# Optimization experiments

Hardware: AMD Instinct MI355X
Metric: run time of the kernel (lower is better)

The kernel has to match this reference:

```python
import jax, jax.numpy as jnp
import numpy as np


def setup_inputs() -> dict:
    key = jax.random.key(0)
    kq, kk = jax.random.split(key)
    B, Q, K, D = 32, 512, 512, 1024
    queries = jax.random.normal(kq, (B, Q, D), dtype=jnp.float32)
    keys = jax.random.normal(kk, (B, K, D), dtype=jnp.float32)
    # ProbabilityConverter learned scalars (is_temperature=True, is_bias=True)
    temperature = jnp.ones((), dtype=jnp.float32)
    bias = jnp.zeros((), dtype=jnp.float32)
    return {"queries": queries, "keys": keys, "temperature": temperature, "bias": bias}


def reference(queries, keys, temperature, bias):
    # Dot scoring: (B, Q, D) x (B, K, D) -> (B, Q, K)
    logits = jnp.einsum("bqd,bkd->bqk", queries, keys)
    # keys.eq(0.0)[:, :, :1].transpose(1, 2): mask positions where first key feature == 0
    key_mask = (keys[:, :, 0] == 0.0)[:, None, :]  # (B, 1, K)
    neg_inf = jnp.array(-jnp.inf, dtype=logits.dtype)
    logits = jnp.where(key_mask, neg_inf, logits)
    # confidence = sigmoid((logsumexp(logits) + bias) * temperature)
    approx_max_logit = jax.nn.logsumexp(logits, axis=-1)  # (B, Q)
    confidence = jax.nn.sigmoid((approx_max_logit + bias) * temperature)
    attn = jax.nn.softmax(logits, axis=-1)  # (B, Q, K)
    return attn, confidence
```

## Files before the change

### kernel.cpp

```cpp
#include <hip/hip_runtime.h>
#include <math.h>
#include <stdint.h>


#define NB 32
#define NQ 512
#define NK 512
#define ND 1024
#define BK 32
#define NT (ND / BK)
#define BM1 64
#define BM4 64
#define TILE_BYTES 65536
#define WS_TILES ((size_t)NB * NT * TILE_BYTES)
#define WS_TOTAL (WS_TILES + (size_t)NB * NK * 4)

typedef __attribute__((ext_vector_type(8))) short short8;
typedef __attribute__((ext_vector_type(4))) float f32x4;

__device__ __forceinline__ void bf_split(float x, unsigned& hbits, float& lo) {
  unsigned u = __float_as_uint(x);
  unsigned r = u + 0x7fffu + ((u >> 16) & 1u);
  hbits = r & 0xffff0000u;
  lo = x - __uint_as_float(hbits);
}
__device__ __forceinline__ unsigned pack_rn(float x0, float x1) {
  unsigned u0 = __float_as_uint(x0), u1 = __float_as_uint(x1);
  unsigned r0 = u0 + 0x7fffu + ((u0 >> 16) & 1u);
  unsigned r1 = u1 + 0x7fffu + ((u1 >> 16) & 1u);
  return (r0 >> 16) | (r1 & 0xffff0000u);
}

__device__ __forceinline__ int lds_off_write(int r, int c4) {
  int slot = ((c4 >> 1) + (r >> 1)) & 3;
  return r * 32 + slot * 8 + (c4 & 1) * 4;
}
__device__ __forceinline__ int lds_off_read(int r, int quad) {
  int slot = (quad + (r >> 1)) & 3;
  return r * 32 + slot * 8;
}

__global__ __launch_bounds__(256)
void convert_k(const float* __restrict__ Kg, unsigned char* __restrict__ ws) {
  const int bx = blockIdx.x;
  const int batch = bx >> 5, kt = bx & 31;
  const float* src = Kg + (size_t)batch * NK * ND + kt * BK;
  unsigned short* hiB = (unsigned short*)(ws + (size_t)bx * TILE_BYTES);
  unsigned short* loB = hiB + 32768 / 2;
  float* maskB = (float*)(ws + WS_TILES) + batch * NK;

#pragma unroll
  for (int i = 0; i < 16; ++i) {
    int idx = threadIdx.x + 256 * i;
    int c = idx >> 3, c4 = idx & 7;
    float4 v = *(const float4*)(src + (size_t)c * ND + c4 * 4);
    unsigned h0, h1, h2, h3;
    float l0, l1, l2, l3;
    bf_split(v.x, h0, l0); bf_split(v.y, h1, l1);
    bf_split(v.z, h2, l2); bf_split(v.w, h3, l3);
    int off = c * 32 + c4 * 4;
    *(uint2*)(&hiB[off]) = make_uint2((h0 >> 16) | h1, (h2 >> 16) | h3);
    *(uint2*)(&loB[off]) = make_uint2(pack_rn(l0, l1), pack_rn(l2, l3));
    if (kt == 0 && c4 == 0) maskB[c] = v.x;
  }
}

__device__ __forceinline__ void stage_a(unsigned short* hiA, unsigned short* loA,
                                        int ar, int ac4, float4 v) {
  unsigned h0, h1, h2, h3;
  float l0, l1, l2, l3;
  bf_split(v.x, h0, l0); bf_split(v.y, h1, l1);
  bf_split(v.z, h2, l2); bf_split(v.w, h3, l3);
  int off = lds_off_write(ar, ac4);
  *(uint2*)(&hiA[off]) = make_uint2((h0 >> 16) | h1, (h2 >> 16) | h3);
  *(uint2*)(&loA[off]) = make_uint2(pack_rn(l0, l1), pack_rn(l2, l3));
}

#define MFMA_BF16 __builtin_amdgcn_mfma_f32_16x16x32_bf16

#define BODY(KT, CURB, NXTB, CUR, NXT)                                         \
  do {                                                                         \
    short8 ahi[4], alo[4];                                                     \
    _Pragma("unroll") for (int mt = 0; mt < 4; ++mt) {                         \
      int off = lds_off_read(mt * 16 + ln15, quad);                            \
      ahi[mt] = *(const short8*)(&sAhi[CUR][off]);                             \
      alo[mt] = *(const short8*)(&sAlo[CUR][off]);                             \
    }                                                                          \
    if ((KT) + 1 < NT) {                                                       \
      const unsigned char* tb = wsB + (size_t)((KT) + 1) * TILE_BYTES;         \
      _Pragma("unroll") for (int nt = 0; nt < 4; ++nt) {                       \
        NXTB[2 * nt]     = *(const float4*)(tb + nt * 1024 + boff);            \
        NXTB[2 * nt + 1] = *(const float4*)(tb + 32768 + nt * 1024 + boff);    \
      }                                                                        \
      stage_a(sAhi[NXT], sAlo[NXT], ar, ac4, pa);                              \
      if ((KT) + 2 < NT)                                                       \
        pa = *(const float4*)(Qp + ((KT) + 2) * BK + (size_t)ar * ND + ac4 * 4);\
    }                                                                          \
    _Pragma("unroll") for (int nt = 0; nt < 4; ++nt) {                         \
      short8 bhi = *(const short8*)(&CURB[2 * nt]);                            \
      short8 blo = *(const short8*)(&CURB[2 * nt + 1]);                        \
      _Pragma("unroll") for (int mt = 0; mt < 4; ++mt) {                       \
        acc[mt][nt] = MFMA_BF16(ahi[mt], bhi, acc[mt][nt], 0, 0, 0);           \
        acc[mt][nt] = MFMA_BF16(ahi[mt], blo, acc[mt][nt], 0, 0, 0);           \
        acc[mt][nt] = MFMA_BF16(alo[mt], bhi, acc[mt][nt], 0, 0, 0);           \
      }                                                                        \
    }                                                                          \
    asm volatile("s_waitcnt lgkmcnt(0)" ::: "memory");                         \
    __builtin_amdgcn_s_barrier();                                              \
  } while (0)

__global__ __launch_bounds__(512, 2)
void attn_fused_v4(const float* __restrict__ Qg,
                   const unsigned char* __restrict__ ws,
                   const float* __restrict__ Tp, const float* __restrict__ Bp,
                   float* __restrict__ attn, float* __restrict__ conf) {
  __shared__ __align__(16) unsigned short sAhi[2][BM4 * BK];
  __shared__ __align__(16) unsigned short sAlo[2][BM4 * BK];
  __shared__ __align__(16) float sRedA[BM4][8];
  __shared__ __align__(16) float sRedB[BM4][8];

  const int tid = threadIdx.x;
  const int g = blockIdx.x;
  const int batch = (g & 7) | (((g >> 3) & 3) << 3);
  const int q0 = (g >> 5) * BM4;
  const int ln = tid & 63, w = tid >> 6;
  const int ln15 = ln & 15, quad = ln >> 4;
  const int col0 = w * 64;

  const float* Qp = Qg + ((size_t)batch * NQ + q0) * ND;
  const unsigned char* wsB = ws + (size_t)batch * NT * TILE_BYTES;
  const float* maskB = (const float*)(ws + WS_TILES) + batch * NK;

  const int boff = (col0 << 6) + (ln15 << 6) + (quad << 4);
  const int ar = tid >> 3, ac4 = tid & 7;

  f32x4 acc[4][4];
#pragma unroll
  for (int mt = 0; mt < 4; ++mt)
#pragma unroll
    for (int nt = 0; nt < 4; ++nt) acc[mt][nt] = (f32x4){0.f, 0.f, 0.f, 0.f};

  float4 a0 = *(const float4*)(Qp + (size_t)ar * ND + ac4 * 4);
  stage_a(sAhi[0], sAlo[0], ar, ac4, a0);
  float4 pa = *(const float4*)(Qp + BK + (size_t)ar * ND + ac4 * 4);
  float4 pbA[8], pbB[8];
#pragma unroll
  for (int nt = 0; nt < 4; ++nt) {
    pbA[2 * nt]     = *(const float4*)(wsB + nt * 1024 + boff);
    pbA[2 * nt + 1] = *(const float4*)(wsB + 32768 + nt * 1024 + boff);
  }
  asm volatile("s_waitcnt lgkmcnt(0)" ::: "memory");
  __builtin_amdgcn_s_barrier();

  for (int kt = 0; kt < NT; kt += 2) {
    BODY(kt, pbA, pbB, 0, 1);
    BODY(kt + 1, pbB, pbA, 1, 0);
  }

  const float NEGINF = -__builtin_inff();
  float rm[4][4];
#pragma unroll
  for (int mt = 0; mt < 4; ++mt)
#pragma unroll
    for (int rg = 0; rg < 4; ++rg) rm[mt][rg] = NEGINF;

#pragma unroll
  for (int nt = 0; nt < 4; ++nt) {
    int col = col0 + nt * 16 + ln15;
    bool msk = (maskB[col] == 0.0f);
#pragma unroll
    for (int mt = 0; mt < 4; ++mt)
#pragma unroll
      for (int rg = 0; rg < 4; ++rg) {
        float v = msk ? NEGINF : acc[mt][nt][rg];
        acc[mt][nt][rg] = v;
        rm[mt][rg] = fmaxf(rm[mt][rg], v);
      }
  }
#pragma unroll
  for (int mt = 0; mt < 4; ++mt)
#pragma unroll
    for (int rg = 0; rg < 4; ++rg) {
      float v = rm[mt][rg];
#pragma unroll
      for (int d = 1; d < 16; d <<= 1) v = fmaxf(v, __shfl_xor(v, d, 64));
      rm[mt][rg] = v;
    }
  if (ln15 == 0) {
#pragma unroll
    for (int mt = 0; mt < 4; ++mt)
#pragma unroll
      for (int rg = 0; rg < 4; ++rg)
        sRedA[mt * 16 + quad * 4 + rg][w] = rm[mt][rg];
  }
  __syncthreads();

  float gmax[4][4], gsum[4][4];
#pragma unroll
  for (int mt = 0; mt < 4; ++mt)
#pragma unroll
    for (int rg = 0; rg < 4; ++rg) {
      int row = mt * 16 + quad * 4 + rg;
      f32x4 p0 = *(const f32x4*)(&sRedA[row][0]);
      f32x4 p1 = *(const f32x4*)(&sRedA[row][4]);
      gmax[mt][rg] = fmaxf(fmaxf(fmaxf(p0[0], p0[1]), fmaxf(p0[2], p0[3])),
                           fmaxf(fmaxf(p1[0], p1[1]), fmaxf(p1[2], p1[3])));
      gsum[mt][rg] = 0.f;
    }

#pragma unroll
  for (int nt = 0; nt < 4; ++nt)
#pragma unroll
    for (int mt = 0; mt < 4; ++mt)
#pragma unroll
      for (int rg = 0; rg < 4; ++rg) {
        float e = __expf(acc[mt][nt][rg] - gmax[mt][rg]);
        acc[mt][nt][rg] = e;
        gsum[mt][rg] += e;
      }
#pragma unroll
  for (int mt = 0; mt < 4; ++mt)
#pragma unroll
    for (int rg = 0; rg < 4; ++rg) {
      float v = gsum[mt][rg];
#pragma unroll
      for (int d = 1; d < 16; d <<= 1) v += __shfl_xor(v, d, 64);
      gsum[mt][rg] = v;
    }
  if (ln15 == 0) {
#pragma unroll
    for (int mt = 0; mt < 4; ++mt)
#pragma unroll
      for (int rg = 0; rg < 4; ++rg)
        sRedB[mt * 16 + quad * 4 + rg][w] = gsum[mt][rg];
  }
  __syncthreads();
#pragma unroll
  for (int mt = 0; mt < 4; ++mt)
#pragma unroll
    for (int rg = 0; rg < 4; ++rg) {
      int row = mt * 16 + quad * 4 + rg;
      f32x4 p0 = *(const f32x4*)(&sRedB[row][0]);
      f32x4 p1 = *(const f32x4*)(&sRedB[row][4]);
      gsum[mt][rg] = (p0[0] + p0[1]) + (p0[2] + p0[3]) +
                     ((p1[0] + p1[1]) + (p1[2] + p1[3]));
    }

  float* outBase = attn + ((size_t)batch * NQ + q0) * NK;
#pragma unroll
  for (int mt = 0; mt < 4; ++mt)
#pragma unroll
    for (int rg = 0; rg < 4; ++rg) {
      int row = mt * 16 + quad * 4 + rg;
      float inv = 1.0f / gsum[mt][rg];
#pragma unroll
      for (int nt = 0; nt < 4; ++nt)
        outBase[(size_t)row * NK + col0 + nt * 16 + ln15] = acc[mt][nt][rg] * inv;
    }

  if (w == 0 && ln15 == 0) {
    float tv = Tp[0], bv = Bp[0];
#pragma unroll
    for (int mt = 0; mt < 4; ++mt)
#pragma unroll
      for (int rg = 0; rg < 4; ++rg) {
        int row = mt * 16 + quad * 4 + rg;
        float lse = gmax[mt][rg] + __logf(gsum[mt][rg]);
        float t = (lse + bv) * tv;
        conf[(size_t)batch * NQ + q0 + row] = 1.0f / (1.0f + __expf(-t));
      }
  }
}

__global__ __launch_bounds__(256, 1)
void attn_fused_v1(const float* __restrict__ Qg, const float* __restrict__ Kg,
                   const float* __restrict__ Tp, const float* __restrict__ Bp,
                   float* __restrict__ attn, float* __restrict__ conf) {
  __shared__ __align__(16) unsigned short sAhi[BM1 * BK];
  __shared__ __align__(16) unsigned short sAlo[BM1 * BK];
  __shared__ __align__(16) unsigned short sBhi[NK * BK];
  __shared__ __align__(16) unsigned short sBlo[NK * BK];
  __shared__ float sRedA[4][BM1];
  __shared__ float sRedB[4][BM1];

  const int tid = threadIdx.x;
  const int g = blockIdx.x;
  const int batch = (g & 7) | (((g >> 3) & 3) << 3);
  const int q0 = (g >> 5) * BM1;
  const int ln = tid & 63, w = tid >> 6;
  const int ln15 = ln & 15, quad = ln >> 4;
  const int wn0 = w * 128;

  const float* Qp = Qg + ((size_t)batch * NQ + q0) * ND;
  const float* Kp = Kg + (size_t)batch * NK * ND;

  f32x4 acc[4][8];
#pragma unroll
  for (int mt = 0; mt < 4; ++mt)
#pragma unroll
    for (int nt = 0; nt < 8; ++nt) acc[mt][nt] = (f32x4){0.f, 0.f, 0.f, 0.f};

  float4 pb[16], pa[2];
#pragma unroll
  for (int i = 0; i < 16; ++i) {
    int idx = tid + 256 * i, r = idx >> 3, c4 = idx & 7;
    pb[i] = *(const float4*)(Kp + (size_t)r * ND + c4 * 4);
  }
#pragma unroll
  for (int i = 0; i < 2; ++i) {
    int idx = tid + 256 * i, r = idx >> 3, c4 = idx & 7;
    pa[i] = *(const float4*)(Qp + (size_t)r * ND + c4 * 4);
  }

  for (int kt = 0; kt < NT; ++kt) {
    if (kt) __syncthreads();
#pragma unroll
    for (int i = 0; i < 2; ++i) {
      int idx = tid + 256 * i, r = idx >> 3, c4 = idx & 7;
      int off = lds_off_write(r, c4);
      unsigned h0, h1, h2, h3; float l0, l1, l2, l3;
      bf_split(pa[i].x, h0, l0); bf_split(pa[i].y, h1, l1);
      bf_split(pa[i].z, h2, l2); bf_split(pa[i].w, h3, l3);
      *(uint2*)(&sAhi[off]) = make_uint2((h0 >> 16) | h1, (h2 >> 16) | h3);
      *(uint2*)(&sAlo[off]) = make_uint2(pack_rn(l0, l1), pack_rn(l2, l3));
    }
#pragma unroll
    for (int i = 0; i < 16; ++i) {
      int idx = tid + 256 * i, r = idx >> 3, c4 = idx & 7;
      int off = lds_off_write(r, c4);
      unsigned h0, h1, h2, h3; float l0, l1, l2, l3;
      bf_split(pb[i].x, h0, l0); bf_split(pb[i].y, h1, l1);
      bf_split(pb[i].z, h2, l2); bf_split(pb[i].w, h3, l3);
      *(uint2*)(&sBhi[off]) = make_uint2((h0 >> 16) | h1, (h2 >> 16) | h3);
      *(uint2*)(&sBlo[off]) = make_uint2(pack_rn(l0, l1), pack_rn(l2, l3));
    }
    __syncthreads();

    if (kt < NT - 1) {
      const float* Kq = Kp + (kt + 1) * BK;
      const float* Qq = Qp + (kt + 1) * BK;
#pragma unroll
      for (int i = 0; i < 16; ++i) {
        int idx = tid + 256 * i, r = idx >> 3, c4 = idx & 7;
        pb[i] = *(const float4*)(Kq + (size_t)r * ND + c4 * 4);
      }
#pragma unroll
      for (int i = 0; i < 2; ++i) {
        int idx = tid + 256 * i, r = idx >> 3, c4 = idx & 7;
        pa[i] = *(const float4*)(Qq + (size_t)r * ND + c4 * 4);
      }
    }

    short8 ahi[4], alo[4];
#pragma unroll
    for (int mt = 0; mt < 4; ++mt) {
      int off = lds_off_read(mt * 16 + ln15, quad);
      ahi[mt] = *(const short8*)(&sAhi[off]);
      alo[mt] = *(const short8*)(&sAlo[off]);
    }
#pragma unroll
    for (int nt = 0; nt < 8; ++nt) {
      int off = lds_off_read(wn0 + nt * 16 + ln15, quad);
      short8 bhi = *(const short8*)(&sBhi[off]);
      short8 blo = *(const short8*)(&sBlo[off]);
#pragma unroll
      for (int mt = 0; mt < 4; ++mt) {
        acc[mt][nt] = MFMA_BF16(ahi[mt], bhi, acc[mt][nt], 0, 0, 0);
        acc[mt][nt] = MFMA_BF16(ahi[mt], blo, acc[mt][nt], 0, 0, 0);
        acc[mt][nt] = MFMA_BF16(alo[mt], bhi, acc[mt][nt], 0, 0, 0);
      }
    }
  }

  const float NEGINF = -__builtin_inff();
  float rm[4][4];
#pragma unroll
  for (int mt = 0; mt < 4; ++mt)
#pragma unroll
    for (int rg = 0; rg < 4; ++rg) rm[mt][rg] = NEGINF;
#pragma unroll
  for (int nt = 0; nt < 8; ++nt) {
    int col = wn0 + nt * 16 + ln15;
    bool msk = (Kp[(size_t)col * ND] == 0.0f);
#pragma unroll
    for (int mt = 0; mt < 4; ++mt)
#pragma unroll
      for (int rg = 0; rg < 4; ++rg) {
        float v = msk ? NEGINF : acc[mt][nt][rg];
        acc[mt][nt][rg] = v;
        rm[mt][rg] = fmaxf(rm[mt][rg], v);
      }
  }
#pragma unroll
  for (int mt = 0; mt < 4; ++mt)
#pragma unroll
    for (int rg = 0; rg < 4; ++rg) {
      float v = rm[mt][rg];
#pragma unroll
      for (int d = 1; d < 16; d <<= 1) v = fmaxf(v, __shfl_xor(v, d, 64));
      rm[mt][rg] = v;
    }
  if (ln15 == 0)
#pragma unroll
    for (int mt = 0; mt < 4; ++mt)
#pragma unroll
      for (int rg = 0; rg < 4; ++rg)
        sRedA[w][mt * 16 + quad * 4 + rg] = rm[mt][rg];
  __syncthreads();

  float gmax[4][4], gsum[4][4];
#pragma unroll
  for (int mt = 0; mt < 4; ++mt)
#pragma unroll
    for (int rg = 0; rg < 4; ++rg) {
      int row = mt * 16 + quad * 4 + rg;
      gmax[mt][rg] = fmaxf(fmaxf(sRedA[0][row], sRedA[1][row]),
                           fmaxf(sRedA[2][row], sRedA[3][row]));
      gsum[mt][rg] = 0.f;
    }
#pragma unroll
  for (int nt = 0; nt < 8; ++nt)
#pragma unroll
    for (int mt = 0; mt < 4; ++mt)
#pragma unroll
      for (int rg = 0; rg < 4; ++rg) {
        float e = __expf(acc[mt][nt][rg] - gmax[mt][rg]);
        acc[mt][nt][rg] = e;
        gsum[mt][rg] += e;
      }
#pragma unroll
  for (int mt = 0; mt < 4; ++mt)
#pragma unroll
    for (int rg = 0; rg < 4; ++rg) {
      float v = gsum[mt][rg];
#pragma unroll
      for (int d = 1; d < 16; d <<= 1) v += __shfl_xor(v, d, 64);
      gsum[mt][rg] = v;
    }
  if (ln15 == 0)
#pragma unroll
    for (int mt = 0; mt < 4; ++mt)
#pragma unroll
      for (int rg = 0; rg < 4; ++rg)
        sRedB[w][mt * 16 + quad * 4 + rg] = gsum[mt][rg];
  __syncthreads();
#pragma unroll
  for (int mt = 0; mt < 4; ++mt)
#pragma unroll
    for (int rg = 0; rg < 4; ++rg) {
      int row = mt * 16 + quad * 4 + rg;
      gsum[mt][rg] = sRedB[0][row] + sRedB[1][row] + sRedB[2][row] + sRedB[3][row];
    }

  float* outBase = attn + ((size_t)batch * NQ + q0) * NK;
#pragma unroll
  for (int mt = 0; mt < 4; ++mt)
#pragma unroll
    for (int rg = 0; rg < 4; ++rg) {
      int row = mt * 16 + quad * 4 + rg;
      float inv = 1.0f / gsum[mt][rg];
#pragma unroll
      for (int nt = 0; nt < 8; ++nt)
        outBase[(size_t)row * NK + wn0 + nt * 16 + ln15] = acc[mt][nt][rg] * inv;
    }
  if (w == 0 && ln15 == 0) {
    float tv = Tp[0], bv = Bp[0];
#pragma unroll
    for (int mt = 0; mt < 4; ++mt)
#pragma unroll
      for (int rg = 0; rg < 4; ++rg) {
        int row = mt * 16 + quad * 4 + rg;
        float lse = gmax[mt][rg] + __logf(gsum[mt][rg]);
        float t = (lse + bv) * tv;
        conf[(size_t)batch * NQ + q0 + row] = 1.0f / (1.0f + __expf(-t));
      }
  }
}

extern "C" void kernel_launch(void* const* d_in, const int* in_sizes, int n_in,
                              void* d_out, int out_size, void* d_ws, size_t ws_size,
                              hipStream_t stream) {
  const float* q = (const float*)d_in[0];
  const float* k = (const float*)d_in[1];
  const float* temp = (const float*)d_in[2];
  const float* bias = (const float*)d_in[3];
  float* attn = (float*)d_out;
  float* conf = attn + (size_t)NB * NQ * NK;

  if (ws_size >= WS_TOTAL) {
    hipLaunchKernelGGL(convert_k, dim3(NB * NT), dim3(256), 0, stream,
                       k, (unsigned char*)d_ws);
    hipLaunchKernelGGL(attn_fused_v4, dim3(NB * (NQ / BM4)), dim3(512), 0, stream,
                       q, (const unsigned char*)d_ws, temp, bias, attn, conf);
  } else {
    hipLaunchKernelGGL(attn_fused_v1, dim3(NB * (NQ / BM1)), dim3(256), 0, stream,
                       q, k, temp, bias, attn, conf);
  }
}
```

Before: 212.5 us.

## Stage half of the query tile in LDS to drop per-step barriers

Instead of double-buffering a 32-wide query slice in LDS with a barrier every k-step, the kernel now converts and stages half of the query row block (512 columns, padded stride) at once. That gives two bulk staging phases with only a few syncthreads in total. This removes the per-iteration waitcnt/barrier and the interleaved A staging. In exchange it uses much more LDS (about 130KB for hi/lo), which may cut blocks per CU, and it serialises the staging bursts instead of overlapping them with MFMA work.

```diff
diff --git a/kernel.cpp b/kernel.cpp
--- a/kernel.cpp
+++ b/kernel.cpp
@@ -10,7 +10,8 @@
 #define BK 32
 #define NT (ND / BK)
 #define BM1 64
-#define BM4 64
+#define BM5 64
+#define ASTRIDE 520
 #define TILE_BYTES 65536
 #define WS_TILES ((size_t)NB * NT * TILE_BYTES)
 #define WS_TOTAL (WS_TILES + (size_t)NB * NK * 4)
@@ -65,36 +66,23 @@
   }
 }
 
-__device__ __forceinline__ void stage_a(unsigned short* hiA, unsigned short* loA,
-                                        int ar, int ac4, float4 v) {
-  unsigned h0, h1, h2, h3;
-  float l0, l1, l2, l3;
-  bf_split(v.x, h0, l0); bf_split(v.y, h1, l1);
-  bf_split(v.z, h2, l2); bf_split(v.w, h3, l3);
-  int off = lds_off_write(ar, ac4);
-  *(uint2*)(&hiA[off]) = make_uint2((h0 >> 16) | h1, (h2 >> 16) | h3);
-  *(uint2*)(&loA[off]) = make_uint2(pack_rn(l0, l1), pack_rn(l2, l3));
-}
-
 #define MFMA_BF16 __builtin_amdgcn_mfma_f32_16x16x32_bf16
 
-#define BODY(KT, CURB, NXTB, CUR, NXT)                                         \
+#define BODY5(KT, CURB, NXTB)                                                  \
   do {                                                                         \
-    short8 ahi[4], alo[4];                                                     \
-    _Pragma("unroll") for (int mt = 0; mt < 4; ++mt) {                         \
-      int off = lds_off_read(mt * 16 + ln15, quad);                            \
-      ahi[mt] = *(const short8*)(&sAhi[CUR][off]);                             \
-      alo[mt] = *(const short8*)(&sAlo[CUR][off]);                             \
-    }                                                                          \
     if ((KT) + 1 < NT) {                                                       \
       const unsigned char* tb = wsB + (size_t)((KT) + 1) * TILE_BYTES;         \
       _Pragma("unroll") for (int nt = 0; nt < 4; ++nt) {                       \
         NXTB[2 * nt]     = *(const float4*)(tb + nt * 1024 + boff);            \
         NXTB[2 * nt + 1] = *(const float4*)(tb + 32768 + nt * 1024 + boff);    \
       }                                                                        \
-      stage_a(sAhi[NXT], sAlo[NXT], ar, ac4, pa);                              \
-      if ((KT) + 2 < NT)                                                       \
-        pa = *(const float4*)(Qp + ((KT) + 2) * BK + (size_t)ar * ND + ac4 * 4);\
+    }                                                                          \
+    const int ktL = (KT) & 15;                                                 \
+    short8 ahi[4], alo[4];                                                     \
+    _Pragma("unroll") for (int mt = 0; mt < 4; ++mt) {                         \
+      int off = (mt * 16 + ln15) * ASTRIDE + ktL * 32 + quad * 8;              \
+      ahi[mt] = *(const short8*)(&sAhi[off]);                                  \
+      alo[mt] = *(const short8*)(&sAlo[off]);                                  \
     }                                                                          \
     _Pragma("unroll") for (int nt = 0; nt < 4; ++nt) {                         \
       short8 bhi = *(const short8*)(&CURB[2 * nt]);                            \
@@ -105,24 +93,22 @@
         acc[mt][nt] = MFMA_BF16(alo[mt], bhi, acc[mt][nt], 0, 0, 0);           \
       }                                                                        \
     }                                                                          \
-    asm volatile("s_waitcnt lgkmcnt(0)" ::: "memory");                         \
-    __builtin_amdgcn_s_barrier();                                              \
   } while (0)
 
 __global__ __launch_bounds__(512, 2)
-void attn_fused_v4(const float* __restrict__ Qg,
+void attn_fused_v5(const float* __restrict__ Qg,
                    const unsigned char* __restrict__ ws,
                    const float* __restrict__ Tp, const float* __restrict__ Bp,
                    float* __restrict__ attn, float* __restrict__ conf) {
-  __shared__ __align__(16) unsigned short sAhi[2][BM4 * BK];
-  __shared__ __align__(16) unsigned short sAlo[2][BM4 * BK];
-  __shared__ __align__(16) float sRedA[BM4][8];
-  __shared__ __align__(16) float sRedB[BM4][8];
+  __shared__ __align__(16) unsigned short sAhi[BM5 * ASTRIDE];
+  __shared__ __align__(16) unsigned short sAlo[BM5 * ASTRIDE];
+  __shared__ __align__(16) float sRedA[BM5][8];
+  __shared__ __align__(16) float sRedB[BM5][8];
 
   const int tid = threadIdx.x;
   const int g = blockIdx.x;
   const int batch = (g & 7) | (((g >> 3) & 3) << 3);
-  const int q0 = (g >> 5) * BM4;
+  const int q0 = (g >> 5) * BM5;
   const int ln = tid & 63, w = tid >> 6;
   const int ln15 = ln & 15, quad = ln >> 4;
   const int col0 = w * 64;
@@ -132,7 +118,6 @@
   const float* maskB = (const float*)(ws + WS_TILES) + batch * NK;
 
   const int boff = (col0 << 6) + (ln15 << 6) + (quad << 4);
-  const int ar = tid >> 3, ac4 = tid & 7;
 
   f32x4 acc[4][4];
 #pragma unroll
@@ -140,21 +125,45 @@
 #pragma unroll
     for (int nt = 0; nt < 4; ++nt) acc[mt][nt] = (f32x4){0.f, 0.f, 0.f, 0.f};
 
-  float4 a0 = *(const float4*)(Qp + (size_t)ar * ND + ac4 * 4);
-  stage_a(sAhi[0], sAlo[0], ar, ac4, a0);
-  float4 pa = *(const float4*)(Qp + BK + (size_t)ar * ND + ac4 * 4);
+  auto stage_half = [&](int h) {
+#pragma unroll
+    for (int i = 0; i < 16; ++i) {
+      int idx = tid + 512 * i;
+      int row = idx >> 7, kc4 = idx & 127;
+      float4 v = *(const float4*)(Qp + (size_t)row * ND + h * 512 + kc4 * 4);
+      unsigned h0, h1, h2, h3;
+      float l0, l1, l2, l3;
+      bf_split(v.x, h0, l0); bf_split(v.y, h1, l1);
+      bf_split(v.z, h2, l2); bf_split(v.w, h3, l3);
+      int off = row * ASTRIDE + kc4 * 4;
+      *(uint2*)(&sAhi[off]) = make_uint2((h0 >> 16) | h1, (h2 >> 16) | h3);
+      *(uint2*)(&sAlo[off]) = make_uint2(pack_rn(l0, l1), pack_rn(l2, l3));
+    }
+  };
+
+  stage_half(0);
   float4 pbA[8], pbB[8];
 #pragma unroll
   for (int nt = 0; nt < 4; ++nt) {
     pbA[2 * nt]     = *(const float4*)(wsB + nt * 1024 + boff);
     pbA[2 * nt + 1] = *(const float4*)(wsB + 32768 + nt * 1024 + boff);
   }
-  asm volatile("s_waitcnt lgkmcnt(0)" ::: "memory");
-  __builtin_amdgcn_s_barrier();
-
-  for (int kt = 0; kt < NT; kt += 2) {
-    BODY(kt, pbA, pbB, 0, 1);
-    BODY(kt + 1, pbB, pbA, 1, 0);
+  __syncthreads();
+
+#pragma unroll 1
+  for (int kt = 0; kt < 16; kt += 2) {
+    BODY5(kt, pbA, pbB);
+    BODY5(kt + 1, pbB, pbA);
+  }
+
+  __syncthreads();
+  stage_half(1);
+  __syncthreads();
+
+#pragma unroll 1
+  for (int kt = 16; kt < 32; kt += 2) {
+    BODY5(kt, pbA, pbB);
+    BODY5(kt + 1, pbB, pbA);
   }
 
   const float NEGINF = -__builtin_inff();
@@ -490,7 +499,7 @@
   if (ws_size >= WS_TOTAL) {
     hipLaunchKernelGGL(convert_k, dim3(NB * NT), dim3(256), 0, stream,
                        k, (unsigned char*)d_ws);
-    hipLaunchKernelGGL(attn_fused_v4, dim3(NB * (NQ / BM4)), dim3(512), 0, stream,
+    hipLaunchKernelGGL(attn_fused_v5, dim3(NB * (NQ / BM5)), dim3(512), 0, stream,
                        q, (const unsigned char*)d_ws, temp, bias, attn, conf);
   } else {
     hipLaunchKernelGGL(attn_fused_v1, dim3(NB * (NQ / BM1)), dim3(256), 0, stream,
```

New measurement: 212.6 us. About the same (+0.0%).
